# Kernel optimization log

Hardware: AMD Instinct MI355X
Metric: run time of the kernel (lower is better)

Reference implementation:

```python
import jax, jax.numpy as jnp
import numpy as np

B, S, P, I, H, NF, O = 128, 48, 60, 512, 512, 4, 2  # batch, seq_len, pad_size, input_size, hidden, n_filters, output
INITRANGE = 0.1


def setup_inputs() -> dict:
    key = jax.random.key(0)
    ks = jax.random.split(key, 16)
    u = lambda k, shape: jax.random.uniform(k, shape, jnp.float32, -INITRANGE, INITRANGE)
    return {
        "inputs": jax.random.normal(ks[0], (B, S, P, I), jnp.float32),
        # conv: Conv1d(1,1,kernel=input_size,stride=2) == dot product with a length-I vector + scalar bias
        "conv_w": u(ks[1], (I,)),
        "conv_b": u(ks[2], (1,)),
        # bidirectional single-layer GRU params (PyTorch layout: [3H, in], gate order r,z,n)
        "wih_f": u(ks[3], (3 * H, I)), "whh_f": u(ks[4], (3 * H, H)),
        "bih_f": u(ks[5], (3 * H,)), "bhh_f": u(ks[6], (3 * H,)),
        "wih_b": u(ks[7], (3 * H, I)), "whh_b": u(ks[8], (3 * H, H)),
        "bih_b": u(ks[9], (3 * H,)), "bhh_b": u(ks[10], (3 * H,)),
        # conv2: Conv1d(1,n_filters,kernel=hidden*2) == n_filters dot products over the state vector
        "conv2_w": u(ks[11], (NF, 2 * H)),
        "conv2_b": u(ks[12], (NF,)),
        "lin_w": u(ks[13], (O, NF * 2 * H)),
        "lin_b": u(ks[14], (O,)),
        "batch_size": B,
    }


def _gru_dir(x, wih, whh, bih, bhh, reverse):
    # x: [B,S,I]; PyTorch GRU cell math, gate order (r, z, n)
    xp = jnp.einsum("bsi,gi->bsg", x, wih) + bih  # [B,S,3H], input proj hoisted out of scan

    def step(h, xt):
        hp = h @ whh.T + bhh
        xr, xz, xn = jnp.split(xt, 3, axis=-1)
        hr, hz, hn = jnp.split(hp, 3, axis=-1)
        r = jax.nn.sigmoid(xr + hr)
        z = jax.nn.sigmoid(xz + hz)
        n = jnp.tanh(xn + r * hn)
        h_new = (1.0 - z) * n + z * h
        return h_new, h_new

    h0 = jnp.zeros((x.shape[0], whh.shape[1]), x.dtype)
    _, hs = jax.lax.scan(step, h0, jnp.swapaxes(xp, 0, 1), reverse=reverse)
    return jnp.swapaxes(hs, 0, 1)  # [B,S,H], time-major order preserved


def reference(inputs, conv_w, conv_b, wih_f, whh_f, bih_f, bhh_f,
              wih_b, whh_b, bih_b, bhh_b, conv2_w, conv2_b, lin_w, lin_b, batch_size):
    # --- convolutional_layer: per-(visit,code) scalar score, hardtanh(0,1), weighted sum over codes ---
    alpha = jnp.clip(jnp.einsum("bspi,i->bsp", inputs, conv_w) + conv_b[0], 0.0, 1.0)  # [B,S,P]
    emb = jnp.einsum("bsp,bspi->bsi", alpha, inputs)  # [B,S,I]
    # dropout is identity in eval mode
    # --- bidirectional GRU ---
    hf = _gru_dir(emb, wih_f, whh_f, bih_f, bhh_f, reverse=False)
    hb = _gru_dir(emb, wih_b, whh_b, bih_b, bhh_b, reverse=True)
    states = jnp.concatenate([hf, hb], axis=-1)  # [B,S,2H]
    # --- add_beta_attention: n_filters scores per step, softmax over seq, weighted sum of states ---
    logits = jnp.einsum("bsh,fh->bfs", states, conv2_w) + conv2_b[None, :, None]  # [B,F,S]
    beta = jax.nn.softmax(logits, axis=-1)
    context = jnp.einsum("bfs,bsh->bfh", beta, states).reshape(batch_size, -1)  # [B, F*2H]
    out = jax.nn.softmax(context @ lin_w.T + lin_b, axis=-1)  # [B,O]
    return out, alpha, beta
```

## Files before the change

kernel.cpp:

```cpp
#include <hip/hip_runtime.h>

#define B_ 128
#define S_ 48
#define P_ 60
#define I_ 512
#define H_ 512
#define G3 1536
#define NF_ 4
#define O_ 2

typedef __bf16 bf16x8 __attribute__((ext_vector_type(8)));
typedef float f32x4 __attribute__((ext_vector_type(4)));
typedef unsigned long long u64;

__global__ __launch_bounds__(960) void k_alpha_emb(
    const float* __restrict__ x, const float* __restrict__ cw,
    const float* __restrict__ cb, float* __restrict__ alpha_out,
    __bf16* __restrict__ emb_bf)
{
  int bs   = blockIdx.x;
  int tid  = threadIdx.x;
  int wave = tid >> 6, lane = tid & 63;
  const float* xb = x + (size_t)bs * (P_ * I_);

  float w[8];
  {
    const float4* c4 = (const float4*)(cw + lane * 8);
    float4 a = c4[0], b = c4[1];
    w[0]=a.x; w[1]=a.y; w[2]=a.z; w[3]=a.w; w[4]=b.x; w[5]=b.y; w[6]=b.z; w[7]=b.w;
  }
  float cb0 = cb[0];
  float acc[8] = {0,0,0,0,0,0,0,0};
  __shared__ float part[15][512];

  for (int p = wave; p < P_; p += 15) {
    const float4* xr = (const float4*)(xb + (size_t)p * I_ + lane * 8);
    float4 a = xr[0], b = xr[1];
    float xv[8] = {a.x,a.y,a.z,a.w,b.x,b.y,b.z,b.w};
    float d = 0.f;
    #pragma unroll
    for (int j = 0; j < 8; j++) d += xv[j] * w[j];
    #pragma unroll
    for (int off = 32; off >= 1; off >>= 1) d += __shfl_xor(d, off);
    float al = fminf(fmaxf(d + cb0, 0.f), 1.f);
    if (lane == 0) alpha_out[(size_t)bs * P_ + p] = al;
    #pragma unroll
    for (int j = 0; j < 8; j++) acc[j] += al * xv[j];
  }
  #pragma unroll
  for (int j = 0; j < 8; j++) part[wave][lane * 8 + j] = acc[j];
  __syncthreads();
  if (tid < 512) {
    float s = 0.f;
    #pragma unroll
    for (int wv = 0; wv < 15; wv++) s += part[wv][tid];
    emb_bf[(size_t)bs * I_ + tid] = (__bf16)s;
  }
}

__global__ __launch_bounds__(256) void k_gru_all(
    const float* __restrict__ whh_f, const float* __restrict__ whh_b,
    const float* __restrict__ wih_f, const float* __restrict__ wih_b,
    const float* __restrict__ bhh_f, const float* __restrict__ bhh_b,
    const float* __restrict__ bih_f, const float* __restrict__ bih_b,
    const __bf16* __restrict__ emb,
    u64* __restrict__ hbf,
    float* __restrict__ hs,
    unsigned* __restrict__ bar)
{
  int bid = blockIdx.x;
  int dir = bid >> 6;
  int j0  = (bid & 31) * 16;
  int m0  = ((bid >> 5) & 1) * 64;
  int myi = bid & 31;
  int grp = bid >> 5;
  const float* Whh_d = dir ? whh_b : whh_f;
  const float* Wih_d = dir ? wih_b : wih_f;

  __shared__ __bf16 Ahh[48 * 512];
  __shared__ __bf16 Aih[48 * 512];
  for (int it = threadIdx.x; it < 48 * 64; it += 256) {
    int r = it >> 6, c8 = it & 63;
    int grow = (r >> 4) * H_ + j0 + (r & 15);
    int dst = r * 512 + ((c8 ^ (r & 7)) * 8);
    const float* sh = Whh_d + (size_t)grow * I_ + c8 * 8;
    const float* si = Wih_d + (size_t)grow * I_ + c8 * 8;
    float4 a = *(const float4*)(sh), b = *(const float4*)(sh + 4);
    float4 c = *(const float4*)(si), d = *(const float4*)(si + 4);
    bf16x8 oh, oi;
    oh[0]=(__bf16)a.x; oh[1]=(__bf16)a.y; oh[2]=(__bf16)a.z; oh[3]=(__bf16)a.w;
    oh[4]=(__bf16)b.x; oh[5]=(__bf16)b.y; oh[6]=(__bf16)b.z; oh[7]=(__bf16)b.w;
    oi[0]=(__bf16)c.x; oi[1]=(__bf16)c.y; oi[2]=(__bf16)c.z; oi[3]=(__bf16)c.w;
    oi[4]=(__bf16)d.x; oi[5]=(__bf16)d.y; oi[6]=(__bf16)d.z; oi[7]=(__bf16)d.w;
    *(bf16x8*)(Ahh + dst) = oh;
    *(bf16x8*)(Aih + dst) = oi;
  }
  __syncthreads();

  int wave = threadIdx.x >> 6, lane = threadIdx.x & 63;
  int col = lane & 15, hi = lane >> 4;
  int b = m0 + wave * 16 + col;
  int j = j0 + hi * 4;
  const float* bhh = dir ? bhh_b : bhh_f;
  const float* bih = dir ? bih_b : bih_f;
  float4 bhr = *(const float4*)(bhh + j);
  float4 bhz = *(const float4*)(bhh + H_ + j);
  float4 bhn = *(const float4*)(bhh + 2 * H_ + j);
  float4 bxr = *(const float4*)(bih + j);
  float4 bxz = *(const float4*)(bih + H_ + j);
  float4 bxn = *(const float4*)(bih + 2 * H_ + j);
  float bhhA[3][4] = {{bhr.x,bhr.y,bhr.z,bhr.w},{bhz.x,bhz.y,bhz.z,bhz.w},{bhn.x,bhn.y,bhn.z,bhn.w}};
  float bihA[3][4] = {{bxr.x,bxr.y,bxr.z,bxr.w},{bxz.x,bxz.y,bxz.z,bxz.w},{bxn.x,bxn.y,bxn.z,bxn.w}};
  int rb0 = (0 * 16 + col) * 512, rb1 = (1 * 16 + col) * 512, rb2 = (2 * 16 + col) * 512;
  int csw = col & 7;
  const __bf16* embB = emb + (size_t)b * S_ * I_;

  const size_t STEPBUF = (size_t)2 * B_ * (H_ / 4);
  size_t hoff = ((size_t)dir * B_ + b) * (H_ / 4);

  float hprev[4] = {0.f, 0.f, 0.f, 0.f};

  for (int step = 0; step < S_; ++step) {
    int t = dir ? (S_ - 1 - step) : step;
    const __bf16* erow = embB + (size_t)t * I_;

    bf16x8 eb[16];
    #pragma unroll
    for (int kk = 0; kk < 16; ++kk)
      eb[kk] = *(const bf16x8*)(erow + kk * 32 + hi * 8);

    if (step != 0) {
      if (threadIdx.x < 32) {
        const unsigned* pf = bar + (((unsigned)step * 4 + grp) * 32 + threadIdx.x) * 16;
        while (__hip_atomic_load(pf, __ATOMIC_RELAXED, __HIP_MEMORY_SCOPE_AGENT) == 0u) {}
      }
      __syncthreads();
    }

    const u64* hin = hbf + (size_t)step * STEPBUF + hoff;
    u64 hb[32];
    #pragma unroll
    for (int kk = 0; kk < 16; ++kk) {
      hb[2 * kk]     = __hip_atomic_load(hin + kk * 8 + hi * 2, __ATOMIC_RELAXED,
                                         __HIP_MEMORY_SCOPE_AGENT);
      hb[2 * kk + 1] = __hip_atomic_load(hin + kk * 8 + hi * 2 + 1, __ATOMIC_RELAXED,
                                         __HIP_MEMORY_SCOPE_AGENT);
    }

    f32x4 ah0 = {0,0,0,0}, ah1 = {0,0,0,0}, ah2 = {0,0,0,0};
    f32x4 ax0 = {0,0,0,0}, ax1 = {0,0,0,0}, ax2 = {0,0,0,0};
    #pragma unroll
    for (int kk = 0; kk < 16; ++kk) {
      union { u64 u[2]; bf16x8 v; } bu;
      bu.u[0] = hb[2 * kk];
      bu.u[1] = hb[2 * kk + 1];
      int go = ((kk * 4 + hi) ^ csw) * 8;
      bf16x8 a0 = *(const bf16x8*)(Ahh + rb0 + go);
      bf16x8 a1 = *(const bf16x8*)(Ahh + rb1 + go);
      bf16x8 a2 = *(const bf16x8*)(Ahh + rb2 + go);
      bf16x8 w0 = *(const bf16x8*)(Aih + rb0 + go);
      bf16x8 w1 = *(const bf16x8*)(Aih + rb1 + go);
      bf16x8 w2 = *(const bf16x8*)(Aih + rb2 + go);
      ah0 = __builtin_amdgcn_mfma_f32_16x16x32_bf16(a0, bu.v, ah0, 0, 0, 0);
      ax0 = __builtin_amdgcn_mfma_f32_16x16x32_bf16(w0, eb[kk], ax0, 0, 0, 0);
      ah1 = __builtin_amdgcn_mfma_f32_16x16x32_bf16(a1, bu.v, ah1, 0, 0, 0);
      ax1 = __builtin_amdgcn_mfma_f32_16x16x32_bf16(w1, eb[kk], ax1, 0, 0, 0);
      ah2 = __builtin_amdgcn_mfma_f32_16x16x32_bf16(a2, bu.v, ah2, 0, 0, 0);
      ax2 = __builtin_amdgcn_mfma_f32_16x16x32_bf16(w2, eb[kk], ax2, 0, 0, 0);
    }

    union { u64 u; __bf16 h[4]; } pk;
    #pragma unroll
    for (int r = 0; r < 4; r++) {
      float hr = ah0[r] + bhhA[0][r];
      float hz = ah1[r] + bhhA[1][r];
      float hn = ah2[r] + bhhA[2][r];
      float xr = ax0[r] + bihA[0][r];
      float xz = ax1[r] + bihA[1][r];
      float xn = ax2[r] + bihA[2][r];
      float rg = 1.f / (1.f + __expf(-(xr + hr)));
      float zg = 1.f / (1.f + __expf(-(xz + hz)));
      float ng = tanhf(xn + rg * hn);
      float hnew = (1.f - zg) * ng + zg * hprev[r];
      hprev[r] = hnew;
      pk.h[r] = (__bf16)hnew;
    }

    if (step != S_ - 1) {
      u64* hout = hbf + (size_t)(step + 1) * STEPBUF + hoff;
      __hip_atomic_store(hout + (j0 >> 2) + hi, pk.u, __ATOMIC_RELAXED,
                         __HIP_MEMORY_SCOPE_AGENT);
      __syncthreads();
      if (threadIdx.x == 0)
        __hip_atomic_store(bar + (((unsigned)(step + 1) * 4 + grp) * 32 + myi) * 16,
                           1u, __ATOMIC_RELAXED, __HIP_MEMORY_SCOPE_AGENT);
    }

    float4 hv = {hprev[0], hprev[1], hprev[2], hprev[3]};
    *(float4*)(hs + ((size_t)b * S_ + t) * (2 * H_) + dir * H_ + j) = hv;
  }
}

__global__ __launch_bounds__(256) void k_attn(
    const float* __restrict__ hs, const float* __restrict__ c2w,
    const float* __restrict__ c2b, const float* __restrict__ lin_w,
    const float* __restrict__ lin_b, float* __restrict__ out,
    float* __restrict__ beta_out)
{
  int b = blockIdx.x, tid = threadIdx.x;
  const float* st = hs + (size_t)b * S_ * (2 * H_);
  __shared__ float lg[NF_][S_];
  __shared__ float betas[NF_][S_];
  __shared__ float ctx[NF_ * 2 * H_];
  __shared__ float red[2][4];

  if (tid < NF_ * S_) {
    int f = tid / S_, s = tid - f * S_;
    const float4* sv = (const float4*)(st + (size_t)s * (2 * H_));
    const float4* wv = (const float4*)(c2w + (size_t)f * (2 * H_));
    float a = 0.f;
    for (int k = 0; k < 256; k++) {
      float4 x = sv[k], y = wv[k];
      a += x.x * y.x + x.y * y.y + x.z * y.z + x.w * y.w;
    }
    lg[f][s] = a + c2b[f];
  }
  __syncthreads();

  int wv_ = tid >> 6, ln = tid & 63;
  {
    float v = (ln < S_) ? lg[wv_][ln] : -3.4e38f;
    float m = v;
    #pragma unroll
    for (int off = 32; off >= 1; off >>= 1) m = fmaxf(m, __shfl_xor(m, off));
    float e = (ln < S_) ? __expf(v - m) : 0.f;
    float ssum = e;
    #pragma unroll
    for (int off = 32; off >= 1; off >>= 1) ssum += __shfl_xor(ssum, off);
    if (ln < S_) {
      float bta = e / ssum;
      betas[wv_][ln] = bta;
      beta_out[((size_t)b * NF_ + wv_) * S_ + ln] = bta;
    }
  }
  __syncthreads();

  for (int idx = tid; idx < NF_ * 2 * H_; idx += 256) {
    int f = idx >> 10, h = idx & 1023;
    float a = 0.f;
    for (int s = 0; s < S_; s++) a += betas[f][s] * st[(size_t)s * (2 * H_) + h];
    ctx[idx] = a;
  }
  __syncthreads();

  float p0 = 0.f, p1 = 0.f;
  for (int idx = tid; idx < NF_ * 2 * H_; idx += 256) {
    float c = ctx[idx];
    p0 += c * lin_w[idx];
    p1 += c * lin_w[NF_ * 2 * H_ + idx];
  }
  #pragma unroll
  for (int off = 32; off >= 1; off >>= 1) {
    p0 += __shfl_xor(p0, off);
    p1 += __shfl_xor(p1, off);
  }
  if (ln == 0) { red[0][wv_] = p0; red[1][wv_] = p1; }
  __syncthreads();
  if (tid == 0) {
    float l0 = red[0][0] + red[0][1] + red[0][2] + red[0][3] + lin_b[0];
    float l1 = red[1][0] + red[1][1] + red[1][2] + red[1][3] + lin_b[1];
    float m = fmaxf(l0, l1);
    float e0 = __expf(l0 - m), e1 = __expf(l1 - m);
    float s = e0 + e1;
    out[(size_t)b * O_ + 0] = e0 / s;
    out[(size_t)b * O_ + 1] = e1 / s;
  }
}

extern "C" void kernel_launch(void* const* d_in, const int* in_sizes, int n_in,
                              void* d_out, int out_size, void* d_ws, size_t ws_size,
                              hipStream_t stream) {
  const float* inputs = (const float*)d_in[0];
  const float* conv_w = (const float*)d_in[1];
  const float* conv_b = (const float*)d_in[2];
  const float* wih_f  = (const float*)d_in[3];
  const float* whh_f  = (const float*)d_in[4];
  const float* bih_f  = (const float*)d_in[5];
  const float* bhh_f  = (const float*)d_in[6];
  const float* wih_b  = (const float*)d_in[7];
  const float* whh_b  = (const float*)d_in[8];
  const float* bih_b  = (const float*)d_in[9];
  const float* bhh_b  = (const float*)d_in[10];
  const float* c2w    = (const float*)d_in[11];
  const float* c2b    = (const float*)d_in[12];
  const float* lin_w  = (const float*)d_in[13];
  const float* lin_b  = (const float*)d_in[14];

  float* out   = (float*)d_out;
  float* alpha = out + B_ * O_;
  float* beta  = alpha + (size_t)B_ * S_ * P_;

  char* ws = (char*)d_ws;
  __bf16* emb_bf = (__bf16*)ws;
  float*  hs     = (float*)(ws + 6291456);
  unsigned* bar  = (unsigned*)(ws + 31457280);
  u64*    hbf    = (u64*)(ws + 31858688);

  hipMemsetAsync((void*)bar, 0, 401408 + 262144, stream);
  k_alpha_emb<<<B_ * S_, 960, 0, stream>>>(inputs, conv_w, conv_b, alpha, emb_bf);

  {
    const __bf16* emb_arg = emb_bf;
    void* args[] = {(void*)&whh_f, (void*)&whh_b, (void*)&wih_f, (void*)&wih_b,
                    (void*)&bhh_f, (void*)&bhh_b, (void*)&bih_f, (void*)&bih_b,
                    (void*)&emb_arg, (void*)&hbf, (void*)&hs, (void*)&bar};
    hipLaunchCooperativeKernel((void*)k_gru_all, dim3(128), dim3(256), args, 0, stream);
  }

  k_attn<<<B_, 256, 0, stream>>>(hs, c2w, c2b, lin_w, lin_b, out, beta);
}
```

Before: 578.3 us.

## Fuse alpha/embedding producer into cooperative GRU kernel with per-timestep flags

```diff
diff --git a/kernel.cpp b/kernel.cpp
--- a/kernel.cpp
+++ b/kernel.cpp
@@ -5,7 +5,6 @@
 #define P_ 60
 #define I_ 512
 #define H_ 512
-#define G3 1536
 #define NF_ 4
 #define O_ 2
 
@@ -13,191 +12,242 @@
 typedef float f32x4 __attribute__((ext_vector_type(4)));
 typedef unsigned long long u64;
 
-__global__ __launch_bounds__(960) void k_alpha_emb(
-    const float* __restrict__ x, const float* __restrict__ cw,
-    const float* __restrict__ cb, float* __restrict__ alpha_out,
-    __bf16* __restrict__ emb_bf)
-{
-  int bs   = blockIdx.x;
-  int tid  = threadIdx.x;
-  int wave = tid >> 6, lane = tid & 63;
-  const float* xb = x + (size_t)bs * (P_ * I_);
-
-  float w[8];
-  {
-    const float4* c4 = (const float4*)(cw + lane * 8);
-    float4 a = c4[0], b = c4[1];
-    w[0]=a.x; w[1]=a.y; w[2]=a.z; w[3]=a.w; w[4]=b.x; w[5]=b.y; w[6]=b.z; w[7]=b.w;
-  }
-  float cb0 = cb[0];
-  float acc[8] = {0,0,0,0,0,0,0,0};
-  __shared__ float part[15][512];
-
-  for (int p = wave; p < P_; p += 15) {
-    const float4* xr = (const float4*)(xb + (size_t)p * I_ + lane * 8);
-    float4 a = xr[0], b = xr[1];
-    float xv[8] = {a.x,a.y,a.z,a.w,b.x,b.y,b.z,b.w};
-    float d = 0.f;
-    #pragma unroll
-    for (int j = 0; j < 8; j++) d += xv[j] * w[j];
-    #pragma unroll
-    for (int off = 32; off >= 1; off >>= 1) d += __shfl_xor(d, off);
-    float al = fminf(fmaxf(d + cb0, 0.f), 1.f);
-    if (lane == 0) alpha_out[(size_t)bs * P_ + p] = al;
-    #pragma unroll
-    for (int j = 0; j < 8; j++) acc[j] += al * xv[j];
-  }
-  #pragma unroll
-  for (int j = 0; j < 8; j++) part[wave][lane * 8 + j] = acc[j];
-  __syncthreads();
-  if (tid < 512) {
-    float s = 0.f;
-    #pragma unroll
-    for (int wv = 0; wv < 15; wv++) s += part[wv][tid];
-    emb_bf[(size_t)bs * I_ + tid] = (__bf16)s;
-  }
-}
-
-__global__ __launch_bounds__(256) void k_gru_all(
+__global__ __launch_bounds__(512, 2) void k_fused(
+    const float* __restrict__ inputs, const float* __restrict__ conv_w,
+    const float* __restrict__ conv_b,
     const float* __restrict__ whh_f, const float* __restrict__ whh_b,
     const float* __restrict__ wih_f, const float* __restrict__ wih_b,
     const float* __restrict__ bhh_f, const float* __restrict__ bhh_b,
     const float* __restrict__ bih_f, const float* __restrict__ bih_b,
-    const __bf16* __restrict__ emb,
+    float* __restrict__ alpha_out,
+    unsigned* __restrict__ emb32,
     u64* __restrict__ hbf,
     float* __restrict__ hs,
-    unsigned* __restrict__ bar)
+    unsigned* __restrict__ bar,
+    unsigned* __restrict__ percol)
 {
-  int bid = blockIdx.x;
-  int dir = bid >> 6;
-  int j0  = (bid & 31) * 16;
-  int m0  = ((bid >> 5) & 1) * 64;
-  int myi = bid & 31;
-  int grp = bid >> 5;
-  const float* Whh_d = dir ? whh_b : whh_f;
-  const float* Wih_d = dir ? wih_b : wih_f;
-
   __shared__ __bf16 Ahh[48 * 512];
   __shared__ __bf16 Aih[48 * 512];
-  for (int it = threadIdx.x; it < 48 * 64; it += 256) {
-    int r = it >> 6, c8 = it & 63;
-    int grow = (r >> 4) * H_ + j0 + (r & 15);
-    int dst = r * 512 + ((c8 ^ (r & 7)) * 8);
-    const float* sh = Whh_d + (size_t)grow * I_ + c8 * 8;
-    const float* si = Wih_d + (size_t)grow * I_ + c8 * 8;
-    float4 a = *(const float4*)(sh), b = *(const float4*)(sh + 4);
-    float4 c = *(const float4*)(si), d = *(const float4*)(si + 4);
-    bf16x8 oh, oi;
-    oh[0]=(__bf16)a.x; oh[1]=(__bf16)a.y; oh[2]=(__bf16)a.z; oh[3]=(__bf16)a.w;
-    oh[4]=(__bf16)b.x; oh[5]=(__bf16)b.y; oh[6]=(__bf16)b.z; oh[7]=(__bf16)b.w;
-    oi[0]=(__bf16)c.x; oi[1]=(__bf16)c.y; oi[2]=(__bf16)c.z; oi[3]=(__bf16)c.w;
-    oi[4]=(__bf16)d.x; oi[5]=(__bf16)d.y; oi[6]=(__bf16)d.z; oi[7]=(__bf16)d.w;
-    *(bf16x8*)(Ahh + dst) = oh;
-    *(bf16x8*)(Aih + dst) = oi;
-  }
-  __syncthreads();
-
-  int wave = threadIdx.x >> 6, lane = threadIdx.x & 63;
-  int col = lane & 15, hi = lane >> 4;
-  int b = m0 + wave * 16 + col;
-  int j = j0 + hi * 4;
-  const float* bhh = dir ? bhh_b : bhh_f;
-  const float* bih = dir ? bih_b : bih_f;
-  float4 bhr = *(const float4*)(bhh + j);
-  float4 bhz = *(const float4*)(bhh + H_ + j);
-  float4 bhn = *(const float4*)(bhh + 2 * H_ + j);
-  float4 bxr = *(const float4*)(bih + j);
-  float4 bxz = *(const float4*)(bih + H_ + j);
-  float4 bxn = *(const float4*)(bih + 2 * H_ + j);
-  float bhhA[3][4] = {{bhr.x,bhr.y,bhr.z,bhr.w},{bhz.x,bhz.y,bhz.z,bhz.w},{bhn.x,bhn.y,bhn.z,bhn.w}};
-  float bihA[3][4] = {{bxr.x,bxr.y,bxr.z,bxr.w},{bxz.x,bxz.y,bxz.z,bxz.w},{bxn.x,bxn.y,bxn.z,bxn.w}};
-  int rb0 = (0 * 16 + col) * 512, rb1 = (1 * 16 + col) * 512, rb2 = (2 * 16 + col) * 512;
-  int csw = col & 7;
-  const __bf16* embB = emb + (size_t)b * S_ * I_;
-
-  const size_t STEPBUF = (size_t)2 * B_ * (H_ / 4);
-  size_t hoff = ((size_t)dir * B_ + b) * (H_ / 4);
-
-  float hprev[4] = {0.f, 0.f, 0.f, 0.f};
-
-  for (int step = 0; step < S_; ++step) {
-    int t = dir ? (S_ - 1 - step) : step;
-    const __bf16* erow = embB + (size_t)t * I_;
-
-    bf16x8 eb[16];
-    #pragma unroll
-    for (int kk = 0; kk < 16; ++kk)
-      eb[kk] = *(const bf16x8*)(erow + kk * 32 + hi * 8);
-
-    if (step != 0) {
-      if (threadIdx.x < 32) {
-        const unsigned* pf = bar + (((unsigned)step * 4 + grp) * 32 + threadIdx.x) * 16;
-        while (__hip_atomic_load(pf, __ATOMIC_RELAXED, __HIP_MEMORY_SCOPE_AGENT) == 0u) {}
-      }
+  __shared__ float part2[8][512];
+
+  int bid = blockIdx.x;
+
+  if (bid < 128) {
+    int dir = bid >> 6;
+    int j0  = (bid & 31) * 16;
+    int m0  = ((bid >> 5) & 1) * 64;
+    int myi = bid & 31;
+    int grp = bid >> 5;
+    const float* Whh_d = dir ? whh_b : whh_f;
+    const float* Wih_d = dir ? wih_b : wih_f;
+
+    for (int it = threadIdx.x; it < 48 * 64; it += 512) {
+      int r = it >> 6, c8 = it & 63;
+      int grow = (r >> 4) * H_ + j0 + (r & 15);
+      int dst = r * 512 + ((c8 ^ (r & 7)) * 8);
+      const float* sh = Whh_d + (size_t)grow * I_ + c8 * 8;
+      const float* si = Wih_d + (size_t)grow * I_ + c8 * 8;
+      float4 a = *(const float4*)(sh), b = *(const float4*)(sh + 4);
+      float4 c = *(const float4*)(si), d = *(const float4*)(si + 4);
+      bf16x8 oh, oi;
+      oh[0]=(__bf16)a.x; oh[1]=(__bf16)a.y; oh[2]=(__bf16)a.z; oh[3]=(__bf16)a.w;
+      oh[4]=(__bf16)b.x; oh[5]=(__bf16)b.y; oh[6]=(__bf16)b.z; oh[7]=(__bf16)b.w;
+      oi[0]=(__bf16)c.x; oi[1]=(__bf16)c.y; oi[2]=(__bf16)c.z; oi[3]=(__bf16)c.w;
+      oi[4]=(__bf16)d.x; oi[5]=(__bf16)d.y; oi[6]=(__bf16)d.z; oi[7]=(__bf16)d.w;
+      *(bf16x8*)(Ahh + dst) = oh;
+      *(bf16x8*)(Aih + dst) = oi;
+    }
+    __syncthreads();
+
+    if (threadIdx.x < 256) {
+      int wave = threadIdx.x >> 6, lane = threadIdx.x & 63;
+      int col = lane & 15, hi = lane >> 4;
+      int b = m0 + wave * 16 + col;
+      int j = j0 + hi * 4;
+      const float* bhh = dir ? bhh_b : bhh_f;
+      const float* bih = dir ? bih_b : bih_f;
+      float4 bhr = *(const float4*)(bhh + j);
+      float4 bhz = *(const float4*)(bhh + H_ + j);
+      float4 bhn = *(const float4*)(bhh + 2 * H_ + j);
+      float4 bxr = *(const float4*)(bih + j);
+      float4 bxz = *(const float4*)(bih + H_ + j);
+      float4 bxn = *(const float4*)(bih + 2 * H_ + j);
+      float bhhA[3][4] = {{bhr.x,bhr.y,bhr.z,bhr.w},{bhz.x,bhz.y,bhz.z,bhz.w},{bhn.x,bhn.y,bhn.z,bhn.w}};
+      float bihA[3][4] = {{bxr.x,bxr.y,bxr.z,bxr.w},{bxz.x,bxz.y,bxz.z,bxz.w},{bxn.x,bxn.y,bxn.z,bxn.w}};
+      int rb0 = (0 * 16 + col) * 512, rb1 = (1 * 16 + col) * 512, rb2 = (2 * 16 + col) * 512;
+      int csw = col & 7;
+      const u64* embB64 = (const u64*)emb32 + (size_t)b * S_ * 128;
+
+      const size_t STEPBUF = (size_t)2 * B_ * (H_ / 4);
+      size_t hoff = ((size_t)dir * B_ + b) * (H_ / 4);
+      const u64* hd64 = (const u64*)(percol + 48);
+
+      float hprev[4] = {0.f, 0.f, 0.f, 0.f};
+      int esent = 0;
+
+      for (int step = 0; step < S_; ++step) {
+        int t = dir ? (S_ - 1 - step) : step;
+
+        if (!esent) {
+          u64 hd = __hip_atomic_load(hd64, __ATOMIC_RELAXED, __HIP_MEMORY_SCOPE_AGENT);
+          if (hd == 0x0000000100000001ull) esent = 1;
+          else while (__hip_atomic_load(percol + t, __ATOMIC_RELAXED,
+                                        __HIP_MEMORY_SCOPE_AGENT) < 64u) {}
+        }
+
+        const u64* erow64 = embB64 + (size_t)t * 128;
+        u64 ebu[32];
+        #pragma unroll
+        for (int kk = 0; kk < 16; ++kk) {
+          ebu[2 * kk]     = __hip_atomic_load(erow64 + kk * 8 + hi * 2,
+                                              __ATOMIC_RELAXED, __HIP_MEMORY_SCOPE_AGENT);
+          ebu[2 * kk + 1] = __hip_atomic_load(erow64 + kk * 8 + hi * 2 + 1,
+                                              __ATOMIC_RELAXED, __HIP_MEMORY_SCOPE_AGENT);
+        }
+
+        if (step != 0) {
+          if (threadIdx.x < 32) {
+            const unsigned* pf = bar + (((unsigned)step * 4 + grp) * 32 + threadIdx.x) * 16;
+            while (__hip_atomic_load(pf, __ATOMIC_RELAXED, __HIP_MEMORY_SCOPE_AGENT) == 0u) {}
+          }
+          __syncthreads();
+        }
+
+        const u64* hin = hbf + (size_t)step * STEPBUF + hoff;
+        u64 hb[32];
+        #pragma unroll
+        for (int kk = 0; kk < 16; ++kk) {
+          hb[2 * kk]     = __hip_atomic_load(hin + kk * 8 + hi * 2, __ATOMIC_RELAXED,
+                                             __HIP_MEMORY_SCOPE_AGENT);
+          hb[2 * kk + 1] = __hip_atomic_load(hin + kk * 8 + hi * 2 + 1, __ATOMIC_RELAXED,
+                                             __HIP_MEMORY_SCOPE_AGENT);
+        }
+
+        f32x4 ah0 = {0,0,0,0}, ah1 = {0,0,0,0}, ah2 = {0,0,0,0};
+        f32x4 ax0 = {0,0,0,0}, ax1 = {0,0,0,0}, ax2 = {0,0,0,0};
+        #pragma unroll
+        for (int kk = 0; kk < 16; ++kk) {
+          union { u64 u[2]; bf16x8 v; } bu, eu;
+          bu.u[0] = hb[2 * kk];
+          bu.u[1] = hb[2 * kk + 1];
+          eu.u[0] = ebu[2 * kk];
+          eu.u[1] = ebu[2 * kk + 1];
+          int go = ((kk * 4 + hi) ^ csw) * 8;
+          bf16x8 a0 = *(const bf16x8*)(Ahh + rb0 + go);
+          bf16x8 a1 = *(const bf16x8*)(Ahh + rb1 + go);
+          bf16x8 a2 = *(const bf16x8*)(Ahh + rb2 + go);
+          bf16x8 w0 = *(const bf16x8*)(Aih + rb0 + go);
+          bf16x8 w1 = *(const bf16x8*)(Aih + rb1 + go);
+          bf16x8 w2 = *(const bf16x8*)(Aih + rb2 + go);
+          ah0 = __builtin_amdgcn_mfma_f32_16x16x32_bf16(a0, bu.v, ah0, 0, 0, 0);
+          ax0 = __builtin_amdgcn_mfma_f32_16x16x32_bf16(w0, eu.v, ax0, 0, 0, 0);
+          ah1 = __builtin_amdgcn_mfma_f32_16x16x32_bf16(a1, bu.v, ah1, 0, 0, 0);
+          ax1 = __builtin_amdgcn_mfma_f32_16x16x32_bf16(w1, eu.v, ax1, 0, 0, 0);
+          ah2 = __builtin_amdgcn_mfma_f32_16x16x32_bf16(a2, bu.v, ah2, 0, 0, 0);
+          ax2 = __builtin_amdgcn_mfma_f32_16x16x32_bf16(w2, eu.v, ax2, 0, 0, 0);
+        }
+
+        union { u64 u; __bf16 h[4]; } pk;
+        #pragma unroll
+        for (int r = 0; r < 4; r++) {
+          float hr = ah0[r] + bhhA[0][r];
+          float hz = ah1[r] + bhhA[1][r];
+          float hn = ah2[r] + bhhA[2][r];
+          float xr = ax0[r] + bihA[0][r];
+          float xz = ax1[r] + bihA[1][r];
+          float xn = ax2[r] + bihA[2][r];
+          float rg = 1.f / (1.f + __expf(-(xr + hr)));
+          float zg = 1.f / (1.f + __expf(-(xz + hz)));
+          float ng = tanhf(xn + rg * hn);
+          float hnew = (1.f - zg) * ng + zg * hprev[r];
+          hprev[r] = hnew;
+          pk.h[r] = (__bf16)hnew;
+        }
+
+        if (step != S_ - 1) {
+          u64* hout = hbf + (size_t)(step + 1) * STEPBUF + hoff;
+          __hip_atomic_store(hout + (j0 >> 2) + hi, pk.u, __ATOMIC_RELAXED,
+                             __HIP_MEMORY_SCOPE_AGENT);
+          __syncthreads();
+          if (threadIdx.x == 0)
+            __hip_atomic_store(bar + (((unsigned)(step + 1) * 4 + grp) * 32 + myi) * 16,
+                               1u, __ATOMIC_RELAXED, __HIP_MEMORY_SCOPE_AGENT);
+        }
+
+        float4 hv = {hprev[0], hprev[1], hprev[2], hprev[3]};
+        *(float4*)(hs + ((size_t)b * S_ + t) * (2 * H_) + dir * H_ + j) = hv;
+      }
+    } else {
+      for (int step = 0; step < S_; ++step) {
+        if (step != 0) __syncthreads();
+        if (step != S_ - 1) __syncthreads();
+      }
+    }
+  } else {
+    int bid2 = bid - 128;
+    int half = bid2 >> 6;
+    int blk  = bid2 & 63;
+    int bA   = blk * 2;
+    int wv   = threadIdx.x >> 6, lane = threadIdx.x & 63;
+    int batch = bA + (wv >> 2);
+    int wsub  = wv & 3;
+
+    float w[8];
+    {
+      const float4* c4 = (const float4*)(conv_w + lane * 8);
+      float4 a = c4[0], bq = c4[1];
+      w[0]=a.x; w[1]=a.y; w[2]=a.z; w[3]=a.w; w[4]=bq.x; w[5]=bq.y; w[6]=bq.z; w[7]=bq.w;
+    }
+    float cb0 = conv_b[0];
+
+    for (int c = 0; c < 24; ++c) {
+      int s = half ? (47 - c) : c;
+      const float* xb = inputs + ((size_t)batch * S_ + s) * (P_ * I_);
+
+      float acc[8] = {0,0,0,0,0,0,0,0};
+      for (int p = wsub; p < P_; p += 4) {
+        const float4* xr = (const float4*)(xb + (size_t)p * I_ + lane * 8);
+        float4 a = xr[0], bq = xr[1];
+        float xv[8] = {a.x,a.y,a.z,a.w,bq.x,bq.y,bq.z,bq.w};
+        float d = 0.f;
+        #pragma unroll
+        for (int jj = 0; jj < 8; jj++) d += xv[jj] * w[jj];
+        #pragma unroll
+        for (int off = 32; off >= 1; off >>= 1) d += __shfl_xor(d, off);
+        float al = fminf(fmaxf(d + cb0, 0.f), 1.f);
+        if (lane == 0) alpha_out[((size_t)batch * S_ + s) * P_ + p] = al;
+        #pragma unroll
+        for (int jj = 0; jj < 8; jj++) acc[jj] += al * xv[jj];
+      }
+      #pragma unroll
+      for (int jj = 0; jj < 8; jj++) part2[wv][lane * 8 + jj] = acc[jj];
       __syncthreads();
-    }
-
-    const u64* hin = hbf + (size_t)step * STEPBUF + hoff;
-    u64 hb[32];
-    #pragma unroll
-    for (int kk = 0; kk < 16; ++kk) {
-      hb[2 * kk]     = __hip_atomic_load(hin + kk * 8 + hi * 2, __ATOMIC_RELAXED,
-                                         __HIP_MEMORY_SCOPE_AGENT);
-      hb[2 * kk + 1] = __hip_atomic_load(hin + kk * 8 + hi * 2 + 1, __ATOMIC_RELAXED,
-                                         __HIP_MEMORY_SCOPE_AGENT);
-    }
-
-    f32x4 ah0 = {0,0,0,0}, ah1 = {0,0,0,0}, ah2 = {0,0,0,0};
-    f32x4 ax0 = {0,0,0,0}, ax1 = {0,0,0,0}, ax2 = {0,0,0,0};
-    #pragma unroll
-    for (int kk = 0; kk < 16; ++kk) {
-      union { u64 u[2]; bf16x8 v; } bu;
-      bu.u[0] = hb[2 * kk];
-      bu.u[1] = hb[2 * kk + 1];
-      int go = ((kk * 4 + hi) ^ csw) * 8;
-      bf16x8 a0 = *(const bf16x8*)(Ahh + rb0 + go);
-      bf16x8 a1 = *(const bf16x8*)(Ahh + rb1 + go);
-      bf16x8 a2 = *(const bf16x8*)(Ahh + rb2 + go);
-      bf16x8 w0 = *(const bf16x8*)(Aih + rb0 + go);
-      bf16x8 w1 = *(const bf16x8*)(Aih + rb1 + go);
-      bf16x8 w2 = *(const bf16x8*)(Aih + rb2 + go);
-      ah0 = __builtin_amdgcn_mfma_f32_16x16x32_bf16(a0, bu.v, ah0, 0, 0, 0);
-      ax0 = __builtin_amdgcn_mfma_f32_16x16x32_bf16(w0, eb[kk], ax0, 0, 0, 0);
-      ah1 = __builtin_amdgcn_mfma_f32_16x16x32_bf16(a1, bu.v, ah1, 0, 0, 0);
-      ax1 = __builtin_amdgcn_mfma_f32_16x16x32_bf16(w1, eb[kk], ax1, 0, 0, 0);
-      ah2 = __builtin_amdgcn_mfma_f32_16x16x32_bf16(a2, bu.v, ah2, 0, 0, 0);
-      ax2 = __builtin_amdgcn_mfma_f32_16x16x32_bf16(w2, eb[kk], ax2, 0, 0, 0);
-    }
-
-    union { u64 u; __bf16 h[4]; } pk;
-    #pragma unroll
-    for (int r = 0; r < 4; r++) {
-      float hr = ah0[r] + bhhA[0][r];
-      float hz = ah1[r] + bhhA[1][r];
-      float hn = ah2[r] + bhhA[2][r];
-      float xr = ax0[r] + bihA[0][r];
-      float xz = ax1[r] + bihA[1][r];
-      float xn = ax2[r] + bihA[2][r];
-      float rg = 1.f / (1.f + __expf(-(xr + hr)));
-      float zg = 1.f / (1.f + __expf(-(xz + hz)));
-      float ng = tanhf(xn + rg * hn);
-      float hnew = (1.f - zg) * ng + zg * hprev[r];
-      hprev[r] = hnew;
-      pk.h[r] = (__bf16)hnew;
-    }
-
-    if (step != S_ - 1) {
-      u64* hout = hbf + (size_t)(step + 1) * STEPBUF + hoff;
-      __hip_atomic_store(hout + (j0 >> 2) + hi, pk.u, __ATOMIC_RELAXED,
-                         __HIP_MEMORY_SCOPE_AGENT);
+
+      {
+        int tid = threadIdx.x;
+        int bsel = tid >> 8;
+        int wbase = bsel * 4;
+        int widx = tid & 255;
+        int jb = widx * 2;
+        float s0 = part2[wbase][jb]   + part2[wbase+1][jb]
+                 + part2[wbase+2][jb] + part2[wbase+3][jb];
+        float s1 = part2[wbase][jb+1]   + part2[wbase+1][jb+1]
+                 + part2[wbase+2][jb+1] + part2[wbase+3][jb+1];
+        union { __bf16 h[2]; unsigned u; } up;
+        up.h[0] = (__bf16)s0; up.h[1] = (__bf16)s1;
+        int bout = bA + bsel;
+        __hip_atomic_store(emb32 + ((size_t)bout * S_ + s) * 256 + widx, up.u,
+                           __ATOMIC_RELAXED, __HIP_MEMORY_SCOPE_AGENT);
+      }
       __syncthreads();
-      if (threadIdx.x == 0)
-        __hip_atomic_store(bar + (((unsigned)(step + 1) * 4 + grp) * 32 + myi) * 16,
-                           1u, __ATOMIC_RELAXED, __HIP_MEMORY_SCOPE_AGENT);
-    }
-
-    float4 hv = {hprev[0], hprev[1], hprev[2], hprev[3]};
-    *(float4*)(hs + ((size_t)b * S_ + t) * (2 * H_) + dir * H_ + j) = hv;
+      if (threadIdx.x == 0) {
+        unsigned old = __hip_atomic_fetch_add(percol + s, 1u, __ATOMIC_RELAXED,
+                                              __HIP_MEMORY_SCOPE_AGENT);
+        if (old == 63u && c == 23)
+          __hip_atomic_store(percol + 48 + half, 1u, __ATOMIC_RELAXED,
+                             __HIP_MEMORY_SCOPE_AGENT);
+      }
+    }
   }
 }
 
@@ -301,20 +351,22 @@
   float* beta  = alpha + (size_t)B_ * S_ * P_;
 
   char* ws = (char*)d_ws;
-  __bf16* emb_bf = (__bf16*)ws;
-  float*  hs     = (float*)(ws + 6291456);
-  unsigned* bar  = (unsigned*)(ws + 31457280);
-  u64*    hbf    = (u64*)(ws + 31858688);
+  unsigned* emb32 = (unsigned*)ws;
+  float*  hs      = (float*)(ws + 6291456);
+  unsigned* bar   = (unsigned*)(ws + 31457280);
+  unsigned* percol= (unsigned*)(ws + 31850496);
+  u64*    hbf     = (u64*)(ws + 31858688);
 
   hipMemsetAsync((void*)bar, 0, 401408 + 262144, stream);
-  k_alpha_emb<<<B_ * S_, 960, 0, stream>>>(inputs, conv_w, conv_b, alpha, emb_bf);
 
   {
-    const __bf16* emb_arg = emb_bf;
-    void* args[] = {(void*)&whh_f, (void*)&whh_b, (void*)&wih_f, (void*)&wih_b,
+    float* alpha_arg = alpha;
+    void* args[] = {(void*)&inputs, (void*)&conv_w, (void*)&conv_b,
+                    (void*)&whh_f, (void*)&whh_b, (void*)&wih_f, (void*)&wih_b,
                     (void*)&bhh_f, (void*)&bhh_b, (void*)&bih_f, (void*)&bih_b,
-                    (void*)&emb_arg, (void*)&hbf, (void*)&hs, (void*)&bar};
-    hipLaunchCooperativeKernel((void*)k_gru_all, dim3(128), dim3(256), args, 0, stream);
+                    (void*)&alpha_arg, (void*)&emb32, (void*)&hbf, (void*)&hs,
+                    (void*)&bar, (void*)&percol};
+    hipLaunchCooperativeKernel((void*)k_fused, dim3(256), dim3(512), args, 0, stream);
   }
 
   k_attn<<<B_, 256, 0, stream>>>(hs, c2w, c2b, lin_w, lin_b, out, beta);
```

New measurement: 678.1 us. 17.3% more time.
